# Kernel optimization log

Hardware: AMD Instinct MI355X
Metric: run time of the kernel (lower is better)

## Reference

```python
import jax, jax.numpy as jnp
import numpy as np

B, T, C, H = 2, 4096, 768, 12
HD = C // H  # head dim = 64


def setup_inputs() -> dict:
    key = jax.random.key(0)
    k1, k2, k3 = jax.random.split(key, 3)
    x = jax.random.normal(k1, (B, T, C), dtype=jnp.float32)
    # torch Linear stores weight as [out_features, in_features]
    w_attn = jax.random.normal(k2, (3 * C, C), dtype=jnp.float32) * (1.0 / np.sqrt(C))
    w_proj = jax.random.normal(k3, (C, C), dtype=jnp.float32) * (1.0 / np.sqrt(C))
    return {"x": x, "w_attn": w_attn, "w_proj": w_proj}


def reference(x, w_attn, w_proj):
    Bs, Ts, Cs = x.shape
    qkv = jnp.einsum('btc,oc->bto', x, w_attn)  # [B,T,3C]
    q, k, v = jnp.split(qkv, 3, axis=-1)
    # [B,H,T,HD]
    q = q.reshape(Bs, Ts, H, HD).transpose(0, 2, 1, 3)
    k = k.reshape(Bs, Ts, H, HD).transpose(0, 2, 1, 3)
    v = v.reshape(Bs, Ts, H, HD).transpose(0, 2, 1, 3)
    scores = jnp.einsum('bhqd,bhkd->bhqk', q, k) / jnp.sqrt(jnp.float32(HD))
    causal = jnp.tril(jnp.ones((Ts, Ts), dtype=bool))
    scores = jnp.where(causal[None, None, :, :], scores, -jnp.inf)
    att = jax.nn.softmax(scores, axis=-1)
    out = jnp.einsum('bhqk,bhkd->bhqd', att, v)  # [B,H,T,HD]
    out = out.transpose(0, 2, 1, 3).reshape(Bs, Ts, Cs)
    out = jnp.einsum('btc,oc->bto', out, w_proj)
    return out
```

## Files before the change

### kernel.cpp

```cpp
#include <hip/hip_runtime.h>
#include <hip/hip_bf16.h>
#include <cstdint>
#include <cstddef>

constexpr int B_ = 2, T_ = 4096, C_ = 768, H_ = 12, HD_ = 64;
constexpr int M_ = B_ * T_;
constexpr int NQKV_ = 3 * C_;

typedef __bf16 bf16_t;
typedef __bf16 bf16x8 __attribute__((ext_vector_type(8)));
typedef __bf16 bf16x4 __attribute__((ext_vector_type(4)));
typedef __bf16 bf16x2 __attribute__((ext_vector_type(2)));
typedef float  f32x4  __attribute__((ext_vector_type(4)));
typedef float  f32x16 __attribute__((ext_vector_type(16)));
typedef unsigned int u32;
typedef unsigned int u32x4 __attribute__((ext_vector_type(4)));

typedef const __attribute__((address_space(1))) void* gas_t;
typedef __attribute__((address_space(3))) void* las_t;

#define QSCALE 0.1803368801111204f

static __device__ __forceinline__ u32 pkbf16(float a, float b) {
  bf16x2 t;
  t[0] = (bf16_t)a;
  t[1] = (bf16_t)b;
  return __builtin_bit_cast(u32, t);
}

__global__ void cvt_f32_bf16_v4(const float* __restrict__ s,
                                bf16_t* __restrict__ d, int n4) {
  int i = blockIdx.x * blockDim.x + threadIdx.x;
  const int st = gridDim.x * blockDim.x;
  for (; i < n4; i += st) {
    const float4 v = reinterpret_cast<const float4*>(s)[i];
    bf16x4 o;
    o[0] = (bf16_t)v.x; o[1] = (bf16_t)v.y;
    o[2] = (bf16_t)v.z; o[3] = (bf16_t)v.w;
    reinterpret_cast<bf16x4*>(d)[i] = o;
  }
}

#define GEMM_CORE(Xb, Wb)                                                     \
  __shared__ __align__(16) char lds[32768];                                   \
  const int tid = threadIdx.x, lane = tid & 63, wave = tid >> 6;              \
  const int r16 = lane & 15, g = lane >> 4;                                   \
  const int wr = wave >> 1, wc = wave & 1;                                    \
  const int m0 = blockIdx.y * 128;                                            \
  const int n0 = blockIdx.x * 128;                                            \
  int prow[2], goff[2];                                                       \
  _Pragma("unroll")                                                           \
  for (int i = 0; i < 2; ++i) {                                               \
    const int p = (wave * 2 + i) * 64 + lane;                                 \
    prow[i] = p >> 2;                                                         \
    goff[i] = ((p & 3) ^ (prow[i] & 3)) * 8;                                  \
  }                                                                           \
  auto stage = [&](int buf, int k0) {                                         \
    char* const base = lds + buf * 16384;                                     \
    _Pragma("unroll")                                                         \
    for (int i = 0; i < 2; ++i) {                                             \
      __builtin_amdgcn_global_load_lds(                                       \
          (gas_t)(Xb + (size_t)prow[i] * C_ + k0 + goff[i]),                  \
          (las_t)(base + (wave * 2 + i) * 1024), 16, 0, 0);                   \
      __builtin_amdgcn_global_load_lds(                                       \
          (gas_t)(Wb + (size_t)prow[i] * C_ + k0 + goff[i]),                  \
          (las_t)(base + 8192 + (wave * 2 + i) * 1024), 16, 0, 0);            \
    }                                                                         \
  };                                                                          \
  f32x4 acc[4][4] = {};                                                       \
  const int kswz = (g ^ (r16 & 3)) * 16;                                      \
  stage(0, 0);                                                                \
  __syncthreads();                                                            \
  constexpr int KT = C_ / 32;                                                 \
  for (int kt = 0; kt < KT; ++kt) {                                           \
    if (kt + 1 < KT) stage((kt + 1) & 1, (kt + 1) * 32);                      \
    const char* Ab = lds + (kt & 1) * 16384;                                  \
    const char* Bb = Ab + 8192;                                               \
    bf16x8 a[4], b[4];                                                        \
    _Pragma("unroll")                                                         \
    for (int i = 0; i < 4; ++i)                                               \
      a[i] = *reinterpret_cast<const bf16x8*>(                                \
          Ab + (wr * 64 + i * 16 + r16) * 64 + kswz);                         \
    _Pragma("unroll")                                                         \
    for (int j = 0; j < 4; ++j)                                               \
      b[j] = *reinterpret_cast<const bf16x8*>(                                \
          Bb + (wc * 64 + j * 16 + r16) * 64 + kswz);                         \
    _Pragma("unroll")                                                         \
    for (int i = 0; i < 4; ++i)                                               \
      _Pragma("unroll")                                                       \
      for (int j = 0; j < 4; ++j)                                             \
        acc[i][j] = __builtin_amdgcn_mfma_f32_16x16x32_bf16(                  \
            a[i], b[j], acc[i][j], 0, 0, 0);                                  \
    __syncthreads();                                                          \
  }

__global__ __launch_bounds__(256) void gemm_qkv(
    const bf16_t* __restrict__ X, const bf16_t* __restrict__ W,
    bf16_t* __restrict__ Q, bf16_t* __restrict__ K, bf16_t* __restrict__ Vt) {
  GEMM_CORE(X + (size_t)blockIdx.y * 128 * C_,
            W + (size_t)blockIdx.x * 128 * C_)

#pragma unroll
  for (int j = 0; j < 4; ++j) {
    const int col = n0 + wc * 64 + j * 16 + r16;
    const int which = col / C_;
    const int c = col - which * C_;
    const int h = c >> 6, d = c & 63;
#pragma unroll
    for (int i = 0; i < 4; ++i) {
#pragma unroll
      for (int r = 0; r < 4; ++r) {
        const int row = m0 + wr * 64 + i * 16 + g * 4 + r;
        const int bb = row >> 12, t = row & (T_ - 1);
        const float v = acc[i][j][r];
        if (which == 0)
          Q[(((size_t)(bb * H_ + h)) * T_ + t) * HD_ + d] = (bf16_t)(v * QSCALE);
        else if (which == 1)
          K[(((size_t)(bb * H_ + h)) * T_ + t) * HD_ + d] = (bf16_t)v;
        else
          Vt[(((size_t)(bb * H_ + h)) * HD_ + d) * (size_t)T_ + t] = (bf16_t)v;
      }
    }
  }
}

__global__ __launch_bounds__(256) void gemm_proj(
    const bf16_t* __restrict__ A, const bf16_t* __restrict__ W,
    float* __restrict__ Out) {
  GEMM_CORE(A + (size_t)blockIdx.y * 128 * C_,
            W + (size_t)blockIdx.x * 128 * C_)

#pragma unroll
  for (int j = 0; j < 4; ++j) {
    const int col = n0 + wc * 64 + j * 16 + r16;
#pragma unroll
    for (int i = 0; i < 4; ++i)
#pragma unroll
      for (int r = 0; r < 4; ++r) {
        const int row = m0 + wr * 64 + i * 16 + g * 4 + r;
        Out[(size_t)row * C_ + col] = acc[i][j][r];
      }
  }
}

__global__ __launch_bounds__(512) void attn_fwd(
    const bf16_t* __restrict__ Q, const bf16_t* __restrict__ K,
    const bf16_t* __restrict__ Vt, bf16_t* __restrict__ O) {
  __shared__ __align__(16) char lds[33280];
  const int tid = threadIdx.x;
  const int lane = tid & 63, wave = tid >> 6;
  const int wq = wave & 3;
  const int ksw = wave >> 2;
  const int c32 = lane & 31, h = lane >> 5;
  const int bh = blockIdx.x;
  const int y = gridDim.y - 1 - blockIdx.y;
  const int q0w = 128 * y + 32 * wq;

  const bf16_t* Qb = Q + (size_t)bh * T_ * HD_;
  const bf16_t* Kb = K + (size_t)bh * T_ * HD_;
  const bf16_t* Vb = Vt + (size_t)bh * HD_ * T_;

  bf16x8 qf[4];
#pragma unroll
  for (int dg = 0; dg < 4; ++dg)
    qf[dg] = *reinterpret_cast<const bf16x8*>(
        Qb + (size_t)(q0w + c32) * HD_ + dg * 16 + h * 8);

  bf16x8 ones;
#pragma unroll
  for (int q = 0; q < 8; ++q) ones[q] = (bf16_t)1.0f;

  f32x16 o0 = {}, o1 = {};
  f32x16 lac = {};

  const int srow = tid >> 3;
  const int sck = (tid & 7) ^ (srow & 7);

  auto STAGE = [&](int t, int buf) {
    char* const kb = lds + buf * 16384;
    __builtin_amdgcn_global_load_lds(
        (gas_t)(Kb + (size_t)(t * 64 + srow) * HD_ + sck * 8),
        (las_t)(kb + wave * 1024), 16, 0, 0);
    __builtin_amdgcn_global_load_lds(
        (gas_t)(Vb + (size_t)srow * T_ + t * 64 + sck * 8),
        (las_t)(kb + 8192 + wave * 1024), 16, 0, 0);
  };

  const int nt = 2 * y + 2;
  STAGE(0, 0);
  __syncthreads();

  for (int t = 0; t < nt; ++t) {
    if (t + 1 < nt) STAGE(t + 1, (t + 1) & 1);
    const char* kl = lds + (t & 1) * 16384;
    const char* vl = kl + 8192;
    const int kb0 = t * 64 + ksw * 32;
    if (kb0 < q0w + 32) {
      f32x16 s = {};
#pragma unroll
      for (int dg = 0; dg < 4; ++dg) {
        const bf16x8 kf = *reinterpret_cast<const bf16x8*>(
            kl + (ksw * 32 + c32) * 128 + (((dg * 2 + h) ^ (c32 & 7)) << 4));
        s = __builtin_amdgcn_mfma_f32_32x32x16_bf16(kf, qf[dg], s, 0, 0, 0);
      }
      if (kb0 + 31 > q0w) {
        const int qabs = q0w + c32;
        const int kbh = kb0 + 4 * h;
#pragma unroll
        for (int r = 0; r < 16; ++r) {
          if (kbh + (r & 3) + 8 * (r >> 2) > qabs) s[r] = -130.f;
        }
      }
#pragma unroll
      for (int r = 0; r < 16; ++r) s[r] = exp2f(s[r]);
      u32 X0 = pkbf16(s[0], s[1]),  X1 = pkbf16(s[2], s[3]);
      u32 X2 = pkbf16(s[4], s[5]),  X3 = pkbf16(s[6], s[7]);
      u32 X4 = pkbf16(s[8], s[9]),  X5 = pkbf16(s[10], s[11]);
      u32 X6 = pkbf16(s[12], s[13]), X7 = pkbf16(s[14], s[15]);
      const auto a0 = __builtin_amdgcn_permlane32_swap(X0, X2, false, false);
      const auto a1 = __builtin_amdgcn_permlane32_swap(X1, X3, false, false);
      const auto a2 = __builtin_amdgcn_permlane32_swap(X4, X6, false, false);
      const auto a3 = __builtin_amdgcn_permlane32_swap(X5, X7, false, false);
      const u32x4 w1 = {(u32)a0[0], (u32)a1[0], (u32)a0[1], (u32)a1[1]};
      const u32x4 w2 = {(u32)a2[0], (u32)a3[0], (u32)a2[1], (u32)a3[1]};
      const bf16x8 pa1 = __builtin_bit_cast(bf16x8, w1);
      const bf16x8 pa2 = __builtin_bit_cast(bf16x8, w2);
      lac = __builtin_amdgcn_mfma_f32_32x32x16_bf16(pa1, ones, lac, 0, 0, 0);
      lac = __builtin_amdgcn_mfma_f32_32x32x16_bf16(pa2, ones, lac, 0, 0, 0);
#pragma unroll
      for (int dgb = 0; dgb < 2; ++dgb) {
        const int vrow = dgb * 32 + c32;
        const bf16x8 vf0 = *reinterpret_cast<const bf16x8*>(
            vl + vrow * 128 + (((ksw * 4 + h) ^ (c32 & 7)) << 4));
        const bf16x8 vf1 = *reinterpret_cast<const bf16x8*>(
            vl + vrow * 128 + (((ksw * 4 + 2 + h) ^ (c32 & 7)) << 4));
        if (dgb == 0) {
          o0 = __builtin_amdgcn_mfma_f32_32x32x16_bf16(pa1, vf0, o0, 0, 0, 0);
          o0 = __builtin_amdgcn_mfma_f32_32x32x16_bf16(pa2, vf1, o0, 0, 0, 0);
        } else {
          o1 = __builtin_amdgcn_mfma_f32_32x32x16_bf16(pa1, vf0, o1, 0, 0, 0);
          o1 = __builtin_amdgcn_mfma_f32_32x32x16_bf16(pa2, vf1, o1, 0, 0, 0);
        }
      }
    }
    __syncthreads();
  }

  float* const obuf = reinterpret_cast<float*>(lds);
  float* const lbuf = reinterpret_cast<float*>(lds + 32768);
  if (wave >= 4) {
    float* const ob = obuf + (wave - 4) * 2048;
#pragma unroll
    for (int r = 0; r < 16; ++r) {
      const int qr = (r & 3) + 8 * (r >> 2) + 4 * h;
      ob[qr * 64 + c32] = o0[r];
      ob[qr * 64 + 32 + c32] = o1[r];
      if (c32 == 0) lbuf[(wave - 4) * 32 + qr] = lac[r];
    }
  }
  __syncthreads();
  if (wave < 4) {
    const float* const ob = obuf + wave * 2048;
    const float* const lb = lbuf + wave * 32;
    const int b = bh / H_, hh = bh - b * H_;
#pragma unroll
    for (int r = 0; r < 16; ++r) {
      const int qr = (r & 3) + 8 * (r >> 2) + 4 * h;
      const float lt = 1.0f / (lac[r] + lb[qr]);
      const float v0 = o0[r] + ob[qr * 64 + c32];
      const float v1 = o1[r] + ob[qr * 64 + 32 + c32];
      const size_t rowoff = ((size_t)(b * T_ + q0w + qr)) * C_ + hh * HD_;
      O[rowoff + c32] = (bf16_t)(v0 * lt);
      O[rowoff + 32 + c32] = (bf16_t)(v1 * lt);
    }
  }
}

extern "C" void kernel_launch(void* const* d_in, const int* in_sizes, int n_in,
                              void* d_out, int out_size, void* d_ws,
                              size_t ws_size, hipStream_t stream) {
  const float* x  = (const float*)d_in[0];
  const float* wa = (const float*)d_in[1];
  const float* wp = (const float*)d_in[2];
  float* out = (float*)d_out;

  char* ws = (char*)d_ws;
  size_t off = 0;
  auto alloc = [&](size_t bytes) -> char* {
    char* p = ws + off;
    off += (bytes + 255) & ~(size_t)255;
    return p;
  };
  bf16_t* xb  = (bf16_t*)alloc((size_t)M_ * C_ * 2);
  bf16_t* wab = (bf16_t*)alloc((size_t)NQKV_ * C_ * 2);
  bf16_t* wpb = (bf16_t*)alloc((size_t)C_ * C_ * 2);
  bf16_t* Qb  = (bf16_t*)alloc((size_t)B_ * H_ * T_ * HD_ * 2);
  bf16_t* Kb  = (bf16_t*)alloc((size_t)B_ * H_ * T_ * HD_ * 2);
  bf16_t* Vtb = (bf16_t*)alloc((size_t)B_ * H_ * HD_ * T_ * 2);
  bf16_t* Ob  = (bf16_t*)alloc((size_t)M_ * C_ * 2);
  if (off > ws_size) return;

  cvt_f32_bf16_v4<<<512, 256, 0, stream>>>(x, xb, M_ * C_ / 4);
  cvt_f32_bf16_v4<<<512, 256, 0, stream>>>(wa, wab, NQKV_ * C_ / 4);
  cvt_f32_bf16_v4<<<256, 256, 0, stream>>>(wp, wpb, C_ * C_ / 4);

  gemm_qkv<<<dim3(NQKV_ / 128, M_ / 128), 256, 0, stream>>>(xb, wab, Qb, Kb, Vtb);
  attn_fwd<<<dim3(B_ * H_, 32), 512, 0, stream>>>(Qb, Kb, Vtb, Ob);
  gemm_proj<<<dim3(C_ / 128, M_ / 128), 256, 0, stream>>>(Ob, wpb, out);
}
```

Before: 194.7 us.

## Shrink attention blocks to 64 queries and remap grid for causal load balancing

The attention kernel now runs 256-thread blocks covering 64 query rows instead of 512-thread blocks covering 128. KV tiles shrink to 32 keys, and the two wave pairs alternate tiles by parity. The grid becomes 256x6 with a permuted mapping that pairs short and long causal rows (y and 63-y) and staggers heads, to balance work across CUs and raise block count. Smaller LDS use allows more resident blocks, at the cost of more K/V reloads per query and twice as many sync iterations.

```diff
diff --git a/kernel.cpp b/kernel.cpp
--- a/kernel.cpp
+++ b/kernel.cpp
@@ -143,18 +143,23 @@
   }
 }
 
-__global__ __launch_bounds__(512) void attn_fwd(
+__global__ __launch_bounds__(256) void attn_fwd(
     const bf16_t* __restrict__ Q, const bf16_t* __restrict__ K,
     const bf16_t* __restrict__ Vt, bf16_t* __restrict__ O) {
-  __shared__ __align__(16) char lds[33280];
+  __shared__ __align__(16) char lds[16896];
   const int tid = threadIdx.x;
   const int lane = tid & 63, wave = tid >> 6;
-  const int wq = wave & 3;
-  const int ksw = wave >> 2;
+  const int wq = wave & 1;
+  const int phi = wave >> 1;
   const int c32 = lane & 31, h = lane >> 5;
-  const int bh = blockIdx.x;
-  const int y = gridDim.y - 1 - blockIdx.y;
-  const int q0w = 128 * y + 32 * wq;
+
+  const int u = blockIdx.x;
+  const int kk = blockIdx.y;
+  const int fam = kk >> 1;
+  const int a = ((u & 63) + fam * 21) & 63;
+  const int y = (kk & 1) ? 63 - a : a;
+  const int bh = (u >> 6) * 6 + kk;
+  const int q0w = 64 * y + 32 * wq;
 
   const bf16_t* Qb = Q + (size_t)bh * T_ * HD_;
   const bf16_t* Kb = K + (size_t)bh * T_ * HD_;
@@ -173,17 +178,19 @@
   f32x16 o0 = {}, o1 = {};
   f32x16 lac = {};
 
-  const int srow = tid >> 3;
-  const int sck = (tid & 7) ^ (srow & 7);
+  const int krow = tid >> 3;
+  const int kck = (tid & 7) ^ (krow & 7);
+  const int vrow = tid >> 2;
+  const int vck = (tid & 3) ^ ((vrow >> 1) & 3);
 
   auto STAGE = [&](int t, int buf) {
-    char* const kb = lds + buf * 16384;
+    char* const kb = lds + buf * 8192;
     __builtin_amdgcn_global_load_lds(
-        (gas_t)(Kb + (size_t)(t * 64 + srow) * HD_ + sck * 8),
+        (gas_t)(Kb + (size_t)(t * 32 + krow) * HD_ + kck * 8),
         (las_t)(kb + wave * 1024), 16, 0, 0);
     __builtin_amdgcn_global_load_lds(
-        (gas_t)(Vb + (size_t)srow * T_ + t * 64 + sck * 8),
-        (las_t)(kb + 8192 + wave * 1024), 16, 0, 0);
+        (gas_t)(Vb + (size_t)vrow * T_ + t * 32 + vck * 8),
+        (las_t)(kb + 4096 + wave * 1024), 16, 0, 0);
   };
 
   const int nt = 2 * y + 2;
@@ -192,15 +199,15 @@
 
   for (int t = 0; t < nt; ++t) {
     if (t + 1 < nt) STAGE(t + 1, (t + 1) & 1);
-    const char* kl = lds + (t & 1) * 16384;
-    const char* vl = kl + 8192;
-    const int kb0 = t * 64 + ksw * 32;
-    if (kb0 < q0w + 32) {
+    const char* kl = lds + (t & 1) * 8192;
+    const char* vl = kl + 4096;
+    const int kb0 = t * 32;
+    if (((t & 1) == phi) && kb0 < q0w + 32) {
       f32x16 s = {};
 #pragma unroll
       for (int dg = 0; dg < 4; ++dg) {
         const bf16x8 kf = *reinterpret_cast<const bf16x8*>(
-            kl + (ksw * 32 + c32) * 128 + (((dg * 2 + h) ^ (c32 & 7)) << 4));
+            kl + c32 * 128 + (((dg * 2 + h) ^ (c32 & 7)) << 4));
         s = __builtin_amdgcn_mfma_f32_32x32x16_bf16(kf, qf[dg], s, 0, 0, 0);
       }
       if (kb0 + 31 > q0w) {
@@ -229,11 +236,12 @@
       lac = __builtin_amdgcn_mfma_f32_32x32x16_bf16(pa2, ones, lac, 0, 0, 0);
 #pragma unroll
       for (int dgb = 0; dgb < 2; ++dgb) {
-        const int vrow = dgb * 32 + c32;
+        const int vr = dgb * 32 + c32;
+        const int vsw = (c32 >> 1) & 3;
         const bf16x8 vf0 = *reinterpret_cast<const bf16x8*>(
-            vl + vrow * 128 + (((ksw * 4 + h) ^ (c32 & 7)) << 4));
+            vl + vr * 64 + ((h ^ vsw) << 4));
         const bf16x8 vf1 = *reinterpret_cast<const bf16x8*>(
-            vl + vrow * 128 + (((ksw * 4 + 2 + h) ^ (c32 & 7)) << 4));
+            vl + vr * 64 + (((2 + h) ^ vsw) << 4));
         if (dgb == 0) {
           o0 = __builtin_amdgcn_mfma_f32_32x32x16_bf16(pa1, vf0, o0, 0, 0, 0);
           o0 = __builtin_amdgcn_mfma_f32_32x32x16_bf16(pa2, vf1, o0, 0, 0, 0);
@@ -247,21 +255,21 @@
   }
 
   float* const obuf = reinterpret_cast<float*>(lds);
-  float* const lbuf = reinterpret_cast<float*>(lds + 32768);
-  if (wave >= 4) {
-    float* const ob = obuf + (wave - 4) * 2048;
+  float* const lbuf = reinterpret_cast<float*>(lds + 16384);
+  if (phi == 1) {
+    float* const ob = obuf + wq * 2048;
 #pragma unroll
     for (int r = 0; r < 16; ++r) {
       const int qr = (r & 3) + 8 * (r >> 2) + 4 * h;
       ob[qr * 64 + c32] = o0[r];
       ob[qr * 64 + 32 + c32] = o1[r];
-      if (c32 == 0) lbuf[(wave - 4) * 32 + qr] = lac[r];
+      if (c32 == 0) lbuf[wq * 32 + qr] = lac[r];
     }
   }
   __syncthreads();
-  if (wave < 4) {
-    const float* const ob = obuf + wave * 2048;
-    const float* const lb = lbuf + wave * 32;
+  if (phi == 0) {
+    const float* const ob = obuf + wq * 2048;
+    const float* const lb = lbuf + wq * 32;
     const int b = bh / H_, hh = bh - b * H_;
 #pragma unroll
     for (int r = 0; r < 16; ++r) {
@@ -305,6 +313,6 @@
   cvt_f32_bf16_v4<<<256, 256, 0, stream>>>(wp, wpb, C_ * C_ / 4);
 
   gemm_qkv<<<dim3(NQKV_ / 128, M_ / 128), 256, 0, stream>>>(xb, wab, Qb, Kb, Vtb);
-  attn_fwd<<<dim3(B_ * H_, 32), 512, 0, stream>>>(Qb, Kb, Vtb, Ob);
+  attn_fwd<<<dim3(256, 6), 256, 0, stream>>>(Qb, Kb, Vtb, Ob);
   gemm_proj<<<dim3(C_ / 128, M_ / 128), 256, 0, stream>>>(Ob, wpb, out);
 }
```

New measurement: 286.7 us. +47.3%, slower.
